# Optimization experiments

Hardware: AMD Instinct MI355X
Metric: run time of the kernel (lower is better)

## Reference

```python
import jax, jax.numpy as jnp
import numpy as np
import math

CHUNK = 64

def _linear(x, W, b):
    # torch nn.Linear: y = x @ W.T + b
    return jnp.einsum('bsd,ed->bse', x, W) + b

def setup_inputs() -> dict:
    key = jax.random.key(0)
    ks = jax.random.split(key, 10)
    B, S, D = 4, 4096, 512
    scale = 0.02
    inp = {
        'x': jax.random.normal(ks[0], (B, S, D), jnp.float32),
        'base_phases': jax.random.normal(ks[1], (S, D), jnp.float32) * math.pi,
        'Wk': jax.random.normal(ks[2], (D, D), jnp.float32) * scale,
        'bk': jnp.zeros((D,), jnp.float32),
        'Wv': jax.random.normal(ks[3], (D, D), jnp.float32) * scale,
        'bv': jnp.zeros((D,), jnp.float32),
        'Wq': jax.random.normal(ks[4], (D, D), jnp.float32) * scale,
        'bq': jnp.zeros((D,), jnp.float32),
        'Wkm': jax.random.normal(ks[5], (D, D), jnp.float32) * scale,
        'bkm': jnp.zeros((D,), jnp.float32),
        'Wqm': jax.random.normal(ks[6], (D, D), jnp.float32) * scale,
        'bqm': jnp.zeros((D,), jnp.float32),
        'mod_scale': jnp.ones((1,), jnp.float32) * 0.1,
        'ln_g': jnp.ones((D,), jnp.float32),
        'ln_b': jnp.zeros((D,), jnp.float32),
        'Wo': jax.random.normal(ks[7], (D, D), jnp.float32) * scale,
        'bo': jnp.zeros((D,), jnp.float32),
    }
    return inp

def reference(x, base_phases, Wk, bk, Wv, bv, Wq, bq, Wkm, bkm, Wqm, bqm, mod_scale, ln_g, ln_b, Wo, bo):
    B, S, D = x.shape
    bp = base_phases[:S][None]                      # [1,S,D]
    key = _linear(x, Wk, bk)
    value = _linear(x, Wv, bv)
    query = _linear(x, Wq, bq)
    key_phase = bp + _linear(key, Wkm, bkm) * mod_scale
    query_phase = bp + _linear(query, Wqm, bqm) * mod_scale
    bound_real = value * jnp.cos(key_phase)
    bound_imag = value * jnp.sin(key_phase)
    # chunked cumulative memory (S divisible by CHUNK -> no padding)
    nC = S // CHUNK
    br = bound_real.reshape(B, nC, CHUNK, D)
    bi = bound_imag.reshape(B, nC, CHUNK, D)
    qp = query_phase.reshape(B, nC, CHUNK, D)
    mem_real = jnp.cumsum(br, axis=2)
    mem_imag = jnp.cumsum(bi, axis=2)
    retrieved = (mem_real * jnp.cos(qp) + mem_imag * jnp.sin(qp)).reshape(B, S, D)
    retrieved = retrieved / math.sqrt(D)
    # LayerNorm + Linear (to_out)
    mu = jnp.mean(retrieved, axis=-1, keepdims=True)
    var = jnp.mean((retrieved - mu) ** 2, axis=-1, keepdims=True)
    normed = (retrieved - mu) / jnp.sqrt(var + 1e-5) * ln_g + ln_b
    out = _linear(normed, Wo, bo)
    return x + out
```

## Files before the change

### kernel.cpp

```cpp
#include <hip/hip_runtime.h>
#include <hip/hip_bf16.h>


typedef __attribute__((ext_vector_type(8))) short short8;
typedef __attribute__((ext_vector_type(4))) float f32x4;

#define M_TOK   16384
#define DIM     512
#define NCHUNK  64
#define RPAD    520

__device__ __forceinline__ void gll16(const void* g, void* l) {
  __builtin_amdgcn_global_load_lds(
      (const __attribute__((address_space(1))) unsigned int*)g,
      (__attribute__((address_space(3))) unsigned int*)l, 16, 0, 0);
}

__device__ __forceinline__ uint2 pack4bf(float4 v) {
  union { __hip_bfloat16 h[4]; uint2 u; } t;
  t.h[0] = __float2bfloat16(v.x);
  t.h[1] = __float2bfloat16(v.y);
  t.h[2] = __float2bfloat16(v.z);
  t.h[3] = __float2bfloat16(v.w);
  return t.u;
}

__global__ __launch_bounds__(256) void prep_all(
    const float* __restrict__ x, __hip_bfloat16* __restrict__ x_bf,
    const float* __restrict__ Wv, const float* __restrict__ Wo,
    const float* __restrict__ bv,
    const float* __restrict__ Wkm, const float* __restrict__ Wqm,
    const float* __restrict__ Wk, const float* __restrict__ Wq,
    const float* __restrict__ bk, const float* __restrict__ bkm,
    const float* __restrict__ bq, const float* __restrict__ bqm,
    __hip_bfloat16* __restrict__ Wall, float* __restrict__ bc1,
    __hip_bfloat16* __restrict__ Wm_bf, __hip_bfloat16* __restrict__ WT_bf) {
  const int tid = threadIdx.x;
  if (blockIdx.x < 8192) {
    int i = blockIdx.x * 256 + tid;
    ((uint2*)x_bf)[i] = pack4bf(((const float4*)x)[i]);
    return;
  }
  const int b = blockIdx.x - 8192;
  if (b < 512) {
    int m = b >> 8;
    int idx = ((b & 255) * 256 + tid) * 4;
    const float* src = m ? Wo : Wv;
    __hip_bfloat16* dst = Wall + (m ? (size_t)1536 * 512 : 0);
    ((uint2*)dst)[idx >> 2] = pack4bf(*(const float4*)(src + idx));
    int t = b * 256 + tid;
    if (t < 512) bc1[t] = bv[t];
  } else if (b < 1024) {
    int bb = b - 512;
    int m = bb >> 8;
    int idx = ((bb & 255) * 256 + tid) * 4;
    const float* src = m ? Wqm : Wkm;
    ((uint2*)(Wm_bf + (size_t)m * 262144))[idx >> 2] =
        pack4bf(*(const float4*)(src + idx));
  } else if (b < 1152) {
    __shared__ float tile[64][65];
    int bb = b - 1024;
    int z = bb >> 6;
    int tl = bb & 63;
    int tr = tl >> 3, tc = tl & 7;
    const float* src = z ? Wq : Wk;
#pragma unroll
    for (int i = 0; i < 4; i++) {
      int r = (tid >> 4) + 16 * i;
      int c4 = (tid & 15) * 4;
      float4 v = *(const float4*)(src + (size_t)(tr * 64 + r) * 512 +
                                  tc * 64 + c4);
      tile[r][c4 + 0] = v.x;
      tile[r][c4 + 1] = v.y;
      tile[r][c4 + 2] = v.z;
      tile[r][c4 + 3] = v.w;
    }
    __syncthreads();
    int orow = tid >> 2;
    int seg = tid & 3;
    __hip_bfloat16* dst = WT_bf + (size_t)z * 262144 +
                          (size_t)(tc * 64 + orow) * 512 + tr * 64 + seg * 16;
#pragma unroll
    for (int q = 0; q < 4; q++) {
      float4 v;
      v.x = tile[seg * 16 + q * 4 + 0][orow];
      v.y = tile[seg * 16 + q * 4 + 1][orow];
      v.z = tile[seg * 16 + q * 4 + 2][orow];
      v.w = tile[seg * 16 + q * 4 + 3][orow];
      *(uint2*)(dst + q * 4) = pack4bf(v);
    }
  } else {
    int row = (b - 1152) * 4 + (tid >> 6);
    int lane = tid & 63;
    int z = row >> 9;
    int i = row & 511;
    const float* Wm = z ? Wqm : Wkm;
    const float* b0 = z ? bq : bk;
    const float* bm = z ? bqm : bkm;
    const float4* w4 = (const float4*)(Wm + (size_t)i * 512 + lane * 8);
    const float4* v4 = (const float4*)(b0 + lane * 8);
    float4 w0 = w4[0], w1 = w4[1], c0 = v4[0], c1 = v4[1];
    float acc = w0.x * c0.x + w0.y * c0.y + w0.z * c0.z + w0.w * c0.w +
                w1.x * c1.x + w1.y * c1.y + w1.z * c1.z + w1.w * c1.w;
#pragma unroll
    for (int off = 32; off; off >>= 1) acc += __shfl_xor(acc, off, 64);
    if (lane == 0) bc1[512 + z * 512 + i] = acc + bm[i];
  }
}

__global__ __launch_bounds__(256) void gemm_bt(
    const __hip_bfloat16* __restrict__ A, int lda,
    const __hip_bfloat16* __restrict__ Bt,
    const float* __restrict__ bias,
    __hip_bfloat16* __restrict__ Cout, int ldc) {
  constexpr int K = 512, BK = 32;
  __shared__ __align__(16) __hip_bfloat16 As[128 * BK];
  __shared__ __align__(16) __hip_bfloat16 Bs[128 * BK];

  const int tid  = threadIdx.x;
  const int lane = tid & 63;
  const int w    = tid >> 6;
  const int wm   = w >> 1;
  const int wn   = w & 1;
  const int m0   = blockIdx.y * 128;
  const int n0   = blockIdx.x * 128;

  const int rS0    = (w * 2 + 0) * 16 + (lane >> 2);
  const int rS1    = (w * 2 + 1) * 16 + (lane >> 2);
  const int kInRow = (lane & 3) * 8;
  const __hip_bfloat16* gA0 = A + (size_t)(m0 + rS0) * lda + kInRow;
  const __hip_bfloat16* gA1 = A + (size_t)(m0 + rS1) * lda + kInRow;
  const __hip_bfloat16* gB0 = Bt + (size_t)(n0 + rS0) * K + kInRow;
  const __hip_bfloat16* gB1 = Bt + (size_t)(n0 + rS1) * K + kInRow;
  char* ldsA0 = (char*)As + (w * 2 + 0) * 1024;
  char* ldsA1 = (char*)As + (w * 2 + 1) * 1024;
  char* ldsB0 = (char*)Bs + (w * 2 + 0) * 1024;
  char* ldsB1 = (char*)Bs + (w * 2 + 1) * 1024;

  f32x4 acc[4][4] = {};

  const int rfA = lane & 15;
  const int rfK = (lane >> 4) * 8;

  for (int kt = 0; kt < K; kt += BK) {
    __syncthreads();
    gll16(gA0 + kt, ldsA0);
    gll16(gA1 + kt, ldsA1);
    gll16(gB0 + kt, ldsB0);
    gll16(gB1 + kt, ldsB1);
    __syncthreads();

    short8 af[4], bf[4];
#pragma unroll
    for (int i = 0; i < 4; i++)
      af[i] = *(const short8*)(As + (wm * 64 + i * 16 + rfA) * BK + rfK);
#pragma unroll
    for (int j = 0; j < 4; j++)
      bf[j] = *(const short8*)(Bs + (wn * 64 + j * 16 + rfA) * BK + rfK);
#pragma unroll
    for (int i = 0; i < 4; i++)
#pragma unroll
      for (int j = 0; j < 4; j++)
        acc[i][j] = __builtin_amdgcn_mfma_f32_16x16x32_bf16(
            af[i], bf[j], acc[i][j], 0, 0, 0);
  }

  const int cq = lane >> 4;
#pragma unroll
  for (int i = 0; i < 4; i++) {
    int row = m0 + wm * 64 + i * 16 + cq * 4;
#pragma unroll
    for (int j = 0; j < 4; j++) {
      int col = n0 + wn * 64 + j * 16 + (lane & 15);
      float bz = bias[col];
#pragma unroll
      for (int r = 0; r < 4; r++) {
        float v = acc[i][j][r] + bz;
        Cout[(size_t)(row + r) * ldc + col] = __float2bfloat16(v);
      }
    }
  }
}

__global__ __launch_bounds__(256) void gemm_compose(
    const __hip_bfloat16* __restrict__ Wm_bf,
    const __hip_bfloat16* __restrict__ WT_bf,
    __hip_bfloat16* __restrict__ Wall) {
  constexpr int K = 512, BK = 32;
  const __hip_bfloat16* A  = Wm_bf + (size_t)blockIdx.z * 262144;
  const __hip_bfloat16* Bt = WT_bf + (size_t)blockIdx.z * 262144;
  __hip_bfloat16* C = Wall + (size_t)(512 + blockIdx.z * 512) * 512;
  __shared__ __align__(16) __hip_bfloat16 As[128 * BK];
  __shared__ __align__(16) __hip_bfloat16 Bs[128 * BK];

  const int tid  = threadIdx.x;
  const int lane = tid & 63;
  const int w    = tid >> 6;
  const int wm   = w >> 1;
  const int wn   = w & 1;
  const int m0   = blockIdx.y * 128;
  const int n0   = blockIdx.x * 128;

  const int rS0    = (w * 2 + 0) * 16 + (lane >> 2);
  const int rS1    = (w * 2 + 1) * 16 + (lane >> 2);
  const int kInRow = (lane & 3) * 8;
  const __hip_bfloat16* gA0 = A + (size_t)(m0 + rS0) * K + kInRow;
  const __hip_bfloat16* gA1 = A + (size_t)(m0 + rS1) * K + kInRow;
  const __hip_bfloat16* gB0 = Bt + (size_t)(n0 + rS0) * K + kInRow;
  const __hip_bfloat16* gB1 = Bt + (size_t)(n0 + rS1) * K + kInRow;
  char* ldsA0 = (char*)As + (w * 2 + 0) * 1024;
  char* ldsA1 = (char*)As + (w * 2 + 1) * 1024;
  char* ldsB0 = (char*)Bs + (w * 2 + 0) * 1024;
  char* ldsB1 = (char*)Bs + (w * 2 + 1) * 1024;

  f32x4 acc[4][4] = {};
  const int rfA = lane & 15;
  const int rfK = (lane >> 4) * 8;

  for (int kt = 0; kt < K; kt += BK) {
    __syncthreads();
    gll16(gA0 + kt, ldsA0);
    gll16(gA1 + kt, ldsA1);
    gll16(gB0 + kt, ldsB0);
    gll16(gB1 + kt, ldsB1);
    __syncthreads();

    short8 af[4], bf[4];
#pragma unroll
    for (int i = 0; i < 4; i++)
      af[i] = *(const short8*)(As + (wm * 64 + i * 16 + rfA) * BK + rfK);
#pragma unroll
    for (int j = 0; j < 4; j++)
      bf[j] = *(const short8*)(Bs + (wn * 64 + j * 16 + rfA) * BK + rfK);
#pragma unroll
    for (int i = 0; i < 4; i++)
#pragma unroll
      for (int j = 0; j < 4; j++)
        acc[i][j] = __builtin_amdgcn_mfma_f32_16x16x32_bf16(
            af[i], bf[j], acc[i][j], 0, 0, 0);
  }

  const int cq = lane >> 4;
#pragma unroll
  for (int i = 0; i < 4; i++) {
    int row = m0 + wm * 64 + i * 16 + cq * 4;
#pragma unroll
    for (int j = 0; j < 4; j++) {
      int col = n0 + wn * 64 + j * 16 + (lane & 15);
#pragma unroll
      for (int r = 0; r < 4; r++)
        C[(size_t)(row + r) * 512 + col] = __float2bfloat16(acc[i][j][r]);
    }
  }
}

__global__ __launch_bounds__(512) void fused_pg(
    const __hip_bfloat16* __restrict__ VKQ,
    const float* __restrict__ bp,
    const float* __restrict__ mod_scale,
    const float* __restrict__ ln_g, const float* __restrict__ ln_b,
    const __hip_bfloat16* __restrict__ WoB,
    const float* __restrict__ bo,
    const float* __restrict__ x,
    float* __restrict__ out) {
  __shared__ __hip_bfloat16 R[64 * RPAD];
  const int tid    = threadIdx.x;
  const int blk    = blockIdx.x;
  const int token0 = blk * 64;
  const int sg0    = (blk & (NCHUNK - 1)) * 64;
  const float msc  = mod_scale[0];
  const float inv_sqrt_d = 0.044194173824159216f;

  {
    const int d = tid;
    float mr = 0.f, mi = 0.f;
    const __hip_bfloat16* vb = VKQ + (size_t)token0 * 1536 + d;
    const float* bb = bp + (size_t)sg0 * 512 + d;
#pragma unroll 4
    for (int s = 0; s < 64; ++s) {
      float v  = __bfloat162float(vb[(size_t)s * 1536]);
      float km = __bfloat162float(vb[(size_t)s * 1536 + 512]);
      float qm = __bfloat162float(vb[(size_t)s * 1536 + 1024]);
      float b  = bb[(size_t)s * 512];
      float kp = b + km * msc;
      float qp = b + qm * msc;
      float sk, ck, sq, cq;
      __sincosf(kp, &sk, &ck);
      __sincosf(qp, &sq, &cq);
      mr += v * ck;
      mi += v * sk;
      R[s * RPAD + d] = __float2bfloat16((mr * cq + mi * sq) * inv_sqrt_d);
    }
  }
  __syncthreads();

  {
    const int lane = tid & 63;
    const int wv   = tid >> 6;
    float gj[8], bj[8];
#pragma unroll
    for (int j = 0; j < 8; j++) {
      int col = lane + 64 * j;
      gj[j] = ln_g[col];
      bj[j] = ln_b[col];
    }
    for (int rr = 0; rr < 8; ++rr) {
      int row = wv * 8 + rr;
      float vals[8], sum = 0.f, sq2 = 0.f;
#pragma unroll
      for (int j = 0; j < 8; j++) {
        float v = __bfloat162float(R[row * RPAD + lane + 64 * j]);
        vals[j] = v;
        sum += v;
        sq2 += v * v;
      }
#pragma unroll
      for (int off = 32; off; off >>= 1) {
        sum += __shfl_xor(sum, off, 64);
        sq2 += __shfl_xor(sq2, off, 64);
      }
      float mu   = sum * (1.f / 512.f);
      float var  = sq2 * (1.f / 512.f) - mu * mu;
      float rstd = rsqrtf(var + 1e-5f);
#pragma unroll
      for (int j = 0; j < 8; j++) {
        float nv = (vals[j] - mu) * rstd * gj[j] + bj[j];
        R[row * RPAD + lane + 64 * j] = __float2bfloat16(nv);
      }
    }
  }
  __syncthreads();

  {
    const int lane = tid & 63;
    const int w    = tid >> 6;
    const int rfA  = lane & 15;
    const int rfK  = (lane >> 4) * 8;
    f32x4 acc[4][4] = {};

    for (int kt = 0; kt < 512; kt += 32) {
      short8 af[4], bf[4];
#pragma unroll
      for (int j = 0; j < 4; j++) {
        int col = w * 64 + j * 16 + rfA;
        bf[j] = *(const short8*)(WoB + (size_t)col * 512 + kt + rfK);
      }
#pragma unroll
      for (int i = 0; i < 4; i++)
        af[i] = *(const short8*)(R + (i * 16 + rfA) * RPAD + kt + rfK);
#pragma unroll
      for (int i = 0; i < 4; i++)
#pragma unroll
        for (int j = 0; j < 4; j++)
          acc[i][j] = __builtin_amdgcn_mfma_f32_16x16x32_bf16(
              af[i], bf[j], acc[i][j], 0, 0, 0);
    }

    const int cq = lane >> 4;
    float bz[4];
#pragma unroll
    for (int j = 0; j < 4; j++) bz[j] = bo[w * 64 + j * 16 + (lane & 15)];
#pragma unroll
    for (int i = 0; i < 4; i++) {
      int row = token0 + i * 16 + cq * 4;
#pragma unroll
      for (int j = 0; j < 4; j++) {
        int col = w * 64 + j * 16 + (lane & 15);
#pragma unroll
        for (int r = 0; r < 4; r++) {
          size_t o = (size_t)(row + r) * 512 + col;
          out[o] = acc[i][j][r] + bz[j] + x[o];
        }
      }
    }
  }
}

extern "C" void kernel_launch(void* const* d_in, const int* in_sizes, int n_in,
                              void* d_out, int out_size, void* d_ws,
                              size_t ws_size, hipStream_t stream) {
  const float* x    = (const float*)d_in[0];
  const float* bp   = (const float*)d_in[1];
  const float* Wk   = (const float*)d_in[2];
  const float* bk   = (const float*)d_in[3];
  const float* Wv   = (const float*)d_in[4];
  const float* bv   = (const float*)d_in[5];
  const float* Wq   = (const float*)d_in[6];
  const float* bq   = (const float*)d_in[7];
  const float* Wkm  = (const float*)d_in[8];
  const float* bkm  = (const float*)d_in[9];
  const float* Wqm  = (const float*)d_in[10];
  const float* bqm  = (const float*)d_in[11];
  const float* msc  = (const float*)d_in[12];
  const float* lng  = (const float*)d_in[13];
  const float* lnb  = (const float*)d_in[14];
  const float* Wo   = (const float*)d_in[15];
  const float* bo   = (const float*)d_in[16];
  float* out = (float*)d_out;

  char* ws = (char*)d_ws;
  __hip_bfloat16* x_bf  = (__hip_bfloat16*)ws;  ws += (size_t)M_TOK * DIM * 2;
  __hip_bfloat16* Wall  = (__hip_bfloat16*)ws;  ws += (size_t)2048 * 512 * 2;
  __hip_bfloat16* Wm_bf = (__hip_bfloat16*)ws;  ws += (size_t)2 * 262144 * 2;
  __hip_bfloat16* WT_bf = (__hip_bfloat16*)ws;  ws += (size_t)2 * 262144 * 2;
  float*          bc1   = (float*)ws;           ws += 1536 * 4;
  __hip_bfloat16* VKQ   = (__hip_bfloat16*)ws;  ws += (size_t)M_TOK * 1536 * 2;

  prep_all<<<9600, 256, 0, stream>>>(x, x_bf, Wv, Wo, bv, Wkm, Wqm, Wk, Wq,
                                     bk, bkm, bq, bqm, Wall, bc1, Wm_bf,
                                     WT_bf);
  gemm_compose<<<dim3(4, 4, 2), 256, 0, stream>>>(Wm_bf, WT_bf, Wall);
  gemm_bt<<<dim3(12, 128), 256, 0, stream>>>(x_bf, DIM, Wall, bc1, VKQ, 1536);
  fused_pg<<<256, 512, 0, stream>>>(VKQ, bp, msc, lng, lnb,
                                    Wall + (size_t)1536 * 512, bo, x, out);
}
```

Baseline: 221.7 us.

## Split chunk cumsum across two thread segments with carry fix-up, 1024-thread blocks

The fused phase/LayerNorm/output kernel now runs 1024 threads per block. The 64-token chunk scan is split into two 32-token halves that run in parallel. The first half's running totals go to shared memory, and the second half's rows are then corrected by adding that carry rotated by the query phase. LayerNorm rows and the output-GEMM column tiles are redistributed across the 16 waves. This halves the serial scan length on a grid of only 256 blocks, at the cost of an extra pass with another sincos per element, extra bf16 rounding of the intermediate, and higher register pressure under the 1024-thread launch bound.

```diff
diff --git a/kernel.cpp b/kernel.cpp
--- a/kernel.cpp
+++ b/kernel.cpp
@@ -254,7 +254,7 @@
   }
 }
 
-__global__ __launch_bounds__(512) void fused_pg(
+__global__ __launch_bounds__(1024) void fused_pg(
     const __hip_bfloat16* __restrict__ VKQ,
     const float* __restrict__ bp,
     const float* __restrict__ mod_scale,
@@ -264,20 +264,23 @@
     const float* __restrict__ x,
     float* __restrict__ out) {
   __shared__ __hip_bfloat16 R[64 * RPAD];
+  __shared__ float Tr[512], Ti[512];
   const int tid    = threadIdx.x;
+  const int seg    = tid >> 9;
+  const int d      = tid & 511;
   const int blk    = blockIdx.x;
   const int token0 = blk * 64;
   const int sg0    = (blk & (NCHUNK - 1)) * 64;
   const float msc  = mod_scale[0];
-  const float inv_sqrt_d = 0.044194173824159216f;
+  const float isd  = 0.044194173824159216f;
 
   {
-    const int d = tid;
+    const int s0 = seg * 32;
     float mr = 0.f, mi = 0.f;
-    const __hip_bfloat16* vb = VKQ + (size_t)token0 * 1536 + d;
-    const float* bb = bp + (size_t)sg0 * 512 + d;
+    const __hip_bfloat16* vb = VKQ + (size_t)(token0 + s0) * 1536 + d;
+    const float* bb = bp + (size_t)(sg0 + s0) * 512 + d;
 #pragma unroll 4
-    for (int s = 0; s < 64; ++s) {
+    for (int s = 0; s < 32; ++s) {
       float v  = __bfloat162float(vb[(size_t)s * 1536]);
       float km = __bfloat162float(vb[(size_t)s * 1536 + 512]);
       float qm = __bfloat162float(vb[(size_t)s * 1536 + 1024]);
@@ -289,7 +292,31 @@
       __sincosf(qp, &sq, &cq);
       mr += v * ck;
       mi += v * sk;
-      R[s * RPAD + d] = __float2bfloat16((mr * cq + mi * sq) * inv_sqrt_d);
+      R[(s0 + s) * RPAD + d] = __float2bfloat16((mr * cq + mi * sq) * isd);
+    }
+    if (seg == 0) {
+      Tr[d] = mr;
+      Ti[d] = mi;
+    }
+  }
+  __syncthreads();
+
+  {
+    const int r0 = 32 + seg * 16;
+    const float pr = Tr[d] * isd;
+    const float pi = Ti[d] * isd;
+    const __hip_bfloat16* qb = VKQ + (size_t)(token0 + r0) * 1536 + 1024 + d;
+    const float* bb = bp + (size_t)(sg0 + r0) * 512 + d;
+#pragma unroll 4
+    for (int s = 0; s < 16; ++s) {
+      float qm = __bfloat162float(qb[(size_t)s * 1536]);
+      float b  = bb[(size_t)s * 512];
+      float qp = b + qm * msc;
+      float sq, cq;
+      __sincosf(qp, &sq, &cq);
+      int idx = (r0 + s) * RPAD + d;
+      float v = __bfloat162float(R[idx]) + pr * cq + pi * sq;
+      R[idx] = __float2bfloat16(v);
     }
   }
   __syncthreads();
@@ -304,8 +331,8 @@
       gj[j] = ln_g[col];
       bj[j] = ln_b[col];
     }
-    for (int rr = 0; rr < 8; ++rr) {
-      int row = wv * 8 + rr;
+    for (int rr = 0; rr < 4; ++rr) {
+      int row = wv * 4 + rr;
       float vals[8], sum = 0.f, sq2 = 0.f;
 #pragma unroll
       for (int j = 0; j < 8; j++) {
@@ -336,13 +363,13 @@
     const int w    = tid >> 6;
     const int rfA  = lane & 15;
     const int rfK  = (lane >> 4) * 8;
-    f32x4 acc[4][4] = {};
+    f32x4 acc[4][2] = {};
 
     for (int kt = 0; kt < 512; kt += 32) {
-      short8 af[4], bf[4];
-#pragma unroll
-      for (int j = 0; j < 4; j++) {
-        int col = w * 64 + j * 16 + rfA;
+      short8 af[4], bf[2];
+#pragma unroll
+      for (int j = 0; j < 2; j++) {
+        int col = w * 32 + j * 16 + rfA;
         bf[j] = *(const short8*)(WoB + (size_t)col * 512 + kt + rfK);
       }
 #pragma unroll
@@ -351,21 +378,21 @@
 #pragma unroll
       for (int i = 0; i < 4; i++)
 #pragma unroll
-        for (int j = 0; j < 4; j++)
+        for (int j = 0; j < 2; j++)
           acc[i][j] = __builtin_amdgcn_mfma_f32_16x16x32_bf16(
               af[i], bf[j], acc[i][j], 0, 0, 0);
     }
 
     const int cq = lane >> 4;
-    float bz[4];
-#pragma unroll
-    for (int j = 0; j < 4; j++) bz[j] = bo[w * 64 + j * 16 + (lane & 15)];
+    float bz[2];
+#pragma unroll
+    for (int j = 0; j < 2; j++) bz[j] = bo[w * 32 + j * 16 + (lane & 15)];
 #pragma unroll
     for (int i = 0; i < 4; i++) {
       int row = token0 + i * 16 + cq * 4;
 #pragma unroll
-      for (int j = 0; j < 4; j++) {
-        int col = w * 64 + j * 16 + (lane & 15);
+      for (int j = 0; j < 2; j++) {
+        int col = w * 32 + j * 16 + (lane & 15);
 #pragma unroll
         for (int r = 0; r < 4; r++) {
           size_t o = (size_t)(row + r) * 512 + col;
@@ -411,6 +438,6 @@
                                      WT_bf);
   gemm_compose<<<dim3(4, 4, 2), 256, 0, stream>>>(Wm_bf, WT_bf, Wall);
   gemm_bt<<<dim3(12, 128), 256, 0, stream>>>(x_bf, DIM, Wall, bc1, VKQ, 1536);
-  fused_pg<<<256, 512, 0, stream>>>(VKQ, bp, msc, lng, lnb,
-                                    Wall + (size_t)1536 * 512, bo, x, out);
-}
+  fused_pg<<<256, 1024, 0, stream>>>(VKQ, bp, msc, lng, lnb,
+                                     Wall + (size_t)1536 * 512, bo, x, out);
+}
```

Result: faster. 203.7 us (-8.1%).

## Fuse input projection GEMM into phase/cumsum/LayerNorm/output kernel

Applied to the files above, without the earlier changes.

Removes the separate x-to-bf16 conversion and the large VKQ projection GEMM. Each 1024-thread block now converts its 64 tokens of x into LDS and computes the V, K-phase and Q-phase projections with MFMA directly. The chunk cumsum is done in registers with wave shuffles, and LayerNorm plus the Wo projection run in the same kernel. This avoids writing and re-reading the 16384x1536 bf16 intermediate, at the cost of only 256 blocks, heavy register pressure (the cksk array plus accumulators) and repeated global reads of the weights per block.

```diff
diff --git a/kernel.cpp b/kernel.cpp
--- a/kernel.cpp
+++ b/kernel.cpp
@@ -7,8 +7,7 @@
 
 #define M_TOK   16384
 #define DIM     512
-#define NCHUNK  64
-#define RPAD    520
+#define APAD    520
 
 __device__ __forceinline__ void gll16(const void* g, void* l) {
   __builtin_amdgcn_global_load_lds(
@@ -25,8 +24,21 @@
   return t.u;
 }
 
+__device__ __forceinline__ unsigned packbf2(float a, float b) {
+  union { __hip_bfloat16 h[2]; unsigned u; } t;
+  t.h[0] = __float2bfloat16(a);
+  t.h[1] = __float2bfloat16(b);
+  return t.u;
+}
+
+__device__ __forceinline__ float bflo(unsigned u) {
+  union { unsigned x; float f; } t; t.x = u << 16; return t.f;
+}
+__device__ __forceinline__ float bfhi(unsigned u) {
+  union { unsigned x; float f; } t; t.x = u & 0xffff0000u; return t.f;
+}
+
 __global__ __launch_bounds__(256) void prep_all(
-    const float* __restrict__ x, __hip_bfloat16* __restrict__ x_bf,
     const float* __restrict__ Wv, const float* __restrict__ Wo,
     const float* __restrict__ bv,
     const float* __restrict__ Wkm, const float* __restrict__ Wqm,
@@ -36,12 +48,7 @@
     __hip_bfloat16* __restrict__ Wall, float* __restrict__ bc1,
     __hip_bfloat16* __restrict__ Wm_bf, __hip_bfloat16* __restrict__ WT_bf) {
   const int tid = threadIdx.x;
-  if (blockIdx.x < 8192) {
-    int i = blockIdx.x * 256 + tid;
-    ((uint2*)x_bf)[i] = pack4bf(((const float4*)x)[i]);
-    return;
-  }
-  const int b = blockIdx.x - 8192;
+  const int b = blockIdx.x;
   if (b < 512) {
     int m = b >> 8;
     int idx = ((b & 255) * 256 + tid) * 4;
@@ -63,13 +70,12 @@
     int z = bb >> 6;
     int tl = bb & 63;
     int tr = tl >> 3, tc = tl & 7;
-    const float* src = z ? Wq : Wk;
 #pragma unroll
     for (int i = 0; i < 4; i++) {
       int r = (tid >> 4) + 16 * i;
       int c4 = (tid & 15) * 4;
-      float4 v = *(const float4*)(src + (size_t)(tr * 64 + r) * 512 +
-                                  tc * 64 + c4);
+      float4 v = *(const float4*)((z ? Wq : Wk) +
+                                  (size_t)(tr * 64 + r) * 512 + tc * 64 + c4);
       tile[r][c4 + 0] = v.x;
       tile[r][c4 + 1] = v.y;
       tile[r][c4 + 2] = v.z;
@@ -81,13 +87,13 @@
     __hip_bfloat16* dst = WT_bf + (size_t)z * 262144 +
                           (size_t)(tc * 64 + orow) * 512 + tr * 64 + seg * 16;
 #pragma unroll
-    for (int q = 0; q < 4; q++) {
+    for (int qq = 0; qq < 4; qq++) {
       float4 v;
-      v.x = tile[seg * 16 + q * 4 + 0][orow];
-      v.y = tile[seg * 16 + q * 4 + 1][orow];
-      v.z = tile[seg * 16 + q * 4 + 2][orow];
-      v.w = tile[seg * 16 + q * 4 + 3][orow];
-      *(uint2*)(dst + q * 4) = pack4bf(v);
+      v.x = tile[seg * 16 + qq * 4 + 0][orow];
+      v.y = tile[seg * 16 + qq * 4 + 1][orow];
+      v.z = tile[seg * 16 + qq * 4 + 2][orow];
+      v.w = tile[seg * 16 + qq * 4 + 3][orow];
+      *(uint2*)(dst + qq * 4) = pack4bf(v);
     }
   } else {
     int row = (b - 1152) * 4 + (tid >> 6);
@@ -108,80 +114,6 @@
   }
 }
 
-__global__ __launch_bounds__(256) void gemm_bt(
-    const __hip_bfloat16* __restrict__ A, int lda,
-    const __hip_bfloat16* __restrict__ Bt,
-    const float* __restrict__ bias,
-    __hip_bfloat16* __restrict__ Cout, int ldc) {
-  constexpr int K = 512, BK = 32;
-  __shared__ __align__(16) __hip_bfloat16 As[128 * BK];
-  __shared__ __align__(16) __hip_bfloat16 Bs[128 * BK];
-
-  const int tid  = threadIdx.x;
-  const int lane = tid & 63;
-  const int w    = tid >> 6;
-  const int wm   = w >> 1;
-  const int wn   = w & 1;
-  const int m0   = blockIdx.y * 128;
-  const int n0   = blockIdx.x * 128;
-
-  const int rS0    = (w * 2 + 0) * 16 + (lane >> 2);
-  const int rS1    = (w * 2 + 1) * 16 + (lane >> 2);
-  const int kInRow = (lane & 3) * 8;
-  const __hip_bfloat16* gA0 = A + (size_t)(m0 + rS0) * lda + kInRow;
-  const __hip_bfloat16* gA1 = A + (size_t)(m0 + rS1) * lda + kInRow;
-  const __hip_bfloat16* gB0 = Bt + (size_t)(n0 + rS0) * K + kInRow;
-  const __hip_bfloat16* gB1 = Bt + (size_t)(n0 + rS1) * K + kInRow;
-  char* ldsA0 = (char*)As + (w * 2 + 0) * 1024;
-  char* ldsA1 = (char*)As + (w * 2 + 1) * 1024;
-  char* ldsB0 = (char*)Bs + (w * 2 + 0) * 1024;
-  char* ldsB1 = (char*)Bs + (w * 2 + 1) * 1024;
-
-  f32x4 acc[4][4] = {};
-
-  const int rfA = lane & 15;
-  const int rfK = (lane >> 4) * 8;
-
-  for (int kt = 0; kt < K; kt += BK) {
-    __syncthreads();
-    gll16(gA0 + kt, ldsA0);
-    gll16(gA1 + kt, ldsA1);
-    gll16(gB0 + kt, ldsB0);
-    gll16(gB1 + kt, ldsB1);
-    __syncthreads();
-
-    short8 af[4], bf[4];
-#pragma unroll
-    for (int i = 0; i < 4; i++)
-      af[i] = *(const short8*)(As + (wm * 64 + i * 16 + rfA) * BK + rfK);
-#pragma unroll
-    for (int j = 0; j < 4; j++)
-      bf[j] = *(const short8*)(Bs + (wn * 64 + j * 16 + rfA) * BK + rfK);
-#pragma unroll
-    for (int i = 0; i < 4; i++)
-#pragma unroll
-      for (int j = 0; j < 4; j++)
-        acc[i][j] = __builtin_amdgcn_mfma_f32_16x16x32_bf16(
-            af[i], bf[j], acc[i][j], 0, 0, 0);
-  }
-
-  const int cq = lane >> 4;
-#pragma unroll
-  for (int i = 0; i < 4; i++) {
-    int row = m0 + wm * 64 + i * 16 + cq * 4;
-#pragma unroll
-    for (int j = 0; j < 4; j++) {
-      int col = n0 + wn * 64 + j * 16 + (lane & 15);
-      float bz = bias[col];
-#pragma unroll
-      for (int r = 0; r < 4; r++) {
-        float v = acc[i][j][r] + bz;
-        Cout[(size_t)(row + r) * ldc + col] = __float2bfloat16(v);
-      }
-    }
-  }
-}
-
 __global__ __launch_bounds__(256) void gemm_compose(
     const __hip_bfloat16* __restrict__ Wm_bf,
     const __hip_bfloat16* __restrict__ WT_bf,
@@ -254,49 +186,148 @@
   }
 }
 
-__global__ __launch_bounds__(512) void fused_pg(
-    const __hip_bfloat16* __restrict__ VKQ,
+__device__ __forceinline__ void mfma_pass(
+    const __hip_bfloat16* __restrict__ Alds,
+    const __hip_bfloat16* __restrict__ Bt,
+    int c, int q, int d0, f32x4 acc[4][2]) {
+  const int rfK = q * 8;
+  for (int kt = 0; kt < 512; kt += 32) {
+    short8 af[4], bf[2];
+#pragma unroll
+    for (int j = 0; j < 2; j++)
+      bf[j] = *(const short8*)(Bt + (size_t)(d0 + 16 * j) * 512 + kt + rfK);
+#pragma unroll
+    for (int i = 0; i < 4; i++)
+      af[i] = *(const short8*)(Alds + (i * 16 + c) * APAD + kt + rfK);
+#pragma unroll
+    for (int i = 0; i < 4; i++)
+#pragma unroll
+      for (int j = 0; j < 2; j++)
+        acc[i][j] = __builtin_amdgcn_mfma_f32_16x16x32_bf16(
+            af[i], bf[j], acc[i][j], 0, 0, 0);
+  }
+}
+
+__global__ __launch_bounds__(1024) void fused_all(
+    const float* __restrict__ x,
+    const __hip_bfloat16* __restrict__ Wall,
+    const float* __restrict__ bc1,
     const float* __restrict__ bp,
     const float* __restrict__ mod_scale,
     const float* __restrict__ ln_g, const float* __restrict__ ln_b,
-    const __hip_bfloat16* __restrict__ WoB,
     const float* __restrict__ bo,
-    const float* __restrict__ x,
     float* __restrict__ out) {
-  __shared__ __hip_bfloat16 R[64 * RPAD];
+  __shared__ __hip_bfloat16 At[64 * APAD];
+  __shared__ __hip_bfloat16 R[64 * APAD];
   const int tid    = threadIdx.x;
-  const int blk    = blockIdx.x;
-  const int token0 = blk * 64;
-  const int sg0    = (blk & (NCHUNK - 1)) * 64;
+  const int lane   = tid & 63;
+  const int wv     = tid >> 6;
+  const int q      = lane >> 4;
+  const int c      = lane & 15;
+  const int token0 = blockIdx.x * 64;
+  const int sg0    = (blockIdx.x & 63) * 64;
   const float msc  = mod_scale[0];
-  const float inv_sqrt_d = 0.044194173824159216f;
-
-  {
-    const int d = tid;
-    float mr = 0.f, mi = 0.f;
-    const __hip_bfloat16* vb = VKQ + (size_t)token0 * 1536 + d;
-    const float* bb = bp + (size_t)sg0 * 512 + d;
-#pragma unroll 4
-    for (int s = 0; s < 64; ++s) {
-      float v  = __bfloat162float(vb[(size_t)s * 1536]);
-      float km = __bfloat162float(vb[(size_t)s * 1536 + 512]);
-      float qm = __bfloat162float(vb[(size_t)s * 1536 + 1024]);
-      float b  = bb[(size_t)s * 512];
-      float kp = b + km * msc;
-      float qp = b + qm * msc;
-      float sk, ck, sq, cq;
-      __sincosf(kp, &sk, &ck);
-      __sincosf(qp, &sq, &cq);
-      mr += v * ck;
-      mi += v * sk;
-      R[s * RPAD + d] = __float2bfloat16((mr * cq + mi * sq) * inv_sqrt_d);
+  const float isd  = 0.044194173824159216f;
+  const int d0     = wv * 32 + c;
+
+  {
+    const float4* xs = (const float4*)(x + (size_t)token0 * 512);
+#pragma unroll
+    for (int kc = 0; kc < 8; kc++) {
+      int idx = kc * 1024 + tid;
+      int row = idx >> 7;
+      int col4 = idx & 127;
+      *(uint2*)((char*)At + row * (APAD * 2) + col4 * 8) = pack4bf(xs[idx]);
     }
   }
   __syncthreads();
 
   {
-    const int lane = tid & 63;
-    const int wv   = tid >> 6;
+    f32x4 acc[4][2] = {};
+    mfma_pass(At, Wall + (size_t)1024 * 512, c, q, d0, acc);
+    float bq0 = bc1[1024 + d0], bq1 = bc1[1024 + d0 + 16];
+#pragma unroll
+    for (int i = 0; i < 4; i++)
+#pragma unroll
+      for (int r = 0; r < 4; r++) {
+        int s = i * 16 + q * 4 + r;
+        const float* bprow = bp + (size_t)(sg0 + s) * 512;
+        R[s * APAD + d0] =
+            __float2bfloat16(bprow[d0] + (acc[i][0][r] + bq0) * msc);
+        R[s * APAD + d0 + 16] =
+            __float2bfloat16(bprow[d0 + 16] + (acc[i][1][r] + bq1) * msc);
+      }
+  }
+
+  unsigned cksk[4][2][4];
+  {
+    f32x4 acc[4][2] = {};
+    mfma_pass(At, Wall + (size_t)512 * 512, c, q, d0, acc);
+    float bk0 = bc1[512 + d0], bk1 = bc1[512 + d0 + 16];
+#pragma unroll
+    for (int i = 0; i < 4; i++)
+#pragma unroll
+      for (int r = 0; r < 4; r++) {
+        int s = i * 16 + q * 4 + r;
+        const float* bprow = bp + (size_t)(sg0 + s) * 512;
+        float kp0 = bprow[d0] + (acc[i][0][r] + bk0) * msc;
+        float kp1 = bprow[d0 + 16] + (acc[i][1][r] + bk1) * msc;
+        float s0, c0, s1, c1;
+        __sincosf(kp0, &s0, &c0);
+        __sincosf(kp1, &s1, &c1);
+        cksk[i][0][r] = packbf2(c0, s0);
+        cksk[i][1][r] = packbf2(c1, s1);
+      }
+  }
+
+  {
+    f32x4 acc[4][2] = {};
+    mfma_pass(At, Wall, c, q, d0, acc);
+    float bv0 = bc1[d0], bv1 = bc1[d0 + 16];
+#pragma unroll
+    for (int j = 0; j < 2; j++) {
+      const int d = d0 + 16 * j;
+      const float bvj = j ? bv1 : bv0;
+      float carry_r = 0.f, carry_i = 0.f;
+#pragma unroll
+      for (int i = 0; i < 4; i++) {
+        float br[4], bi[4];
+#pragma unroll
+        for (int r = 0; r < 4; r++) {
+          float v = acc[i][j][r] + bvj;
+          unsigned pk = cksk[i][j][r];
+          br[r] = v * bflo(pk);
+          bi[r] = v * bfhi(pk);
+        }
+        br[1] += br[0]; br[2] += br[1]; br[3] += br[2];
+        bi[1] += bi[0]; bi[2] += bi[1]; bi[3] += bi[2];
+        float Sr = br[3], Si = bi[3];
+        float s0r = __shfl(Sr, c, 64),      s0i = __shfl(Si, c, 64);
+        float s1r = __shfl(Sr, 16 + c, 64), s1i = __shfl(Si, 16 + c, 64);
+        float s2r = __shfl(Sr, 32 + c, 64), s2i = __shfl(Si, 32 + c, 64);
+        float s3r = __shfl(Sr, 48 + c, 64), s3i = __shfl(Si, 48 + c, 64);
+        float Er = (q > 0 ? s0r : 0.f) + (q > 1 ? s1r : 0.f) +
+                   (q > 2 ? s2r : 0.f);
+        float Ei = (q > 0 ? s0i : 0.f) + (q > 1 ? s1i : 0.f) +
+                   (q > 2 ? s2i : 0.f);
+#pragma unroll
+        for (int r = 0; r < 4; r++) {
+          float mr = br[r] + Er + carry_r;
+          float mi = bi[r] + Ei + carry_i;
+          int s = i * 16 + q * 4 + r;
+          float qp = __bfloat162float(R[s * APAD + d]);
+          float sq, cq2;
+          __sincosf(qp, &sq, &cq2);
+          R[s * APAD + d] = __float2bfloat16((mr * cq2 + mi * sq) * isd);
+        }
+        carry_r += s0r + s1r + s2r + s3r;
+        carry_i += s0i + s1i + s2i + s3i;
+      }
+    }
+  }
+  __syncthreads();
+
+  {
     float gj[8], bj[8];
 #pragma unroll
     for (int j = 0; j < 8; j++) {
@@ -304,12 +335,12 @@
       gj[j] = ln_g[col];
       bj[j] = ln_b[col];
     }
-    for (int rr = 0; rr < 8; ++rr) {
-      int row = wv * 8 + rr;
+    for (int rr = 0; rr < 4; ++rr) {
+      int row = wv * 4 + rr;
       float vals[8], sum = 0.f, sq2 = 0.f;
 #pragma unroll
       for (int j = 0; j < 8; j++) {
-        float v = __bfloat162float(R[row * RPAD + lane + 64 * j]);
+        float v = __bfloat162float(R[row * APAD + lane + 64 * j]);
         vals[j] = v;
         sum += v;
         sq2 += v * v;
@@ -325,54 +356,29 @@
 #pragma unroll
       for (int j = 0; j < 8; j++) {
         float nv = (vals[j] - mu) * rstd * gj[j] + bj[j];
-        R[row * RPAD + lane + 64 * j] = __float2bfloat16(nv);
+        R[row * APAD + lane + 64 * j] = __float2bfloat16(nv);
       }
     }
   }
   __syncthreads();
 
   {
-    const int lane = tid & 63;
-    const int w    = tid >> 6;
-    const int rfA  = lane & 15;
-    const int rfK  = (lane >> 4) * 8;
-    f32x4 acc[4][4] = {};
-
-    for (int kt = 0; kt < 512; kt += 32) {
-      short8 af[4], bf[4];
-#pragma unroll
-      for (int j = 0; j < 4; j++) {
-        int col = w * 64 + j * 16 + rfA;
-        bf[j] = *(const short8*)(WoB + (size_t)col * 512 + kt + rfK);
-      }
-#pragma unroll
-      for (int i = 0; i < 4; i++)
-        af[i] = *(const short8*)(R + (i * 16 + rfA) * RPAD + kt + rfK);
-#pragma unroll
-      for (int i = 0; i < 4; i++)
-#pragma unroll
-        for (int j = 0; j < 4; j++)
-          acc[i][j] = __builtin_amdgcn_mfma_f32_16x16x32_bf16(
-              af[i], bf[j], acc[i][j], 0, 0, 0);
-    }
-
-    const int cq = lane >> 4;
-    float bz[4];
-#pragma unroll
-    for (int j = 0; j < 4; j++) bz[j] = bo[w * 64 + j * 16 + (lane & 15)];
-#pragma unroll
-    for (int i = 0; i < 4; i++) {
-      int row = token0 + i * 16 + cq * 4;
-#pragma unroll
-      for (int j = 0; j < 4; j++) {
-        int col = w * 64 + j * 16 + (lane & 15);
+    f32x4 acc[4][2] = {};
+    mfma_pass(R, Wall + (size_t)1536 * 512, c, q, d0, acc);
+    float bz0 = bo[d0], bz1 = bo[d0 + 16];
+#pragma unroll
+    for (int i = 0; i < 4; i++)
+#pragma unroll
+      for (int j = 0; j < 2; j++) {
+        int col = d0 + 16 * j;
+        float bz = j ? bz1 : bz0;
 #pragma unroll
         for (int r = 0; r < 4; r++) {
-          size_t o = (size_t)(row + r) * 512 + col;
-          out[o] = acc[i][j][r] + bz[j] + x[o];
+          int row = token0 + i * 16 + q * 4 + r;
+          size_t o = (size_t)row * 512 + col;
+          out[o] = acc[i][j][r] + bz + x[o];
         }
       }
-    }
   }
 }
 
@@ -399,18 +405,14 @@
   float* out = (float*)d_out;
 
   char* ws = (char*)d_ws;
-  __hip_bfloat16* x_bf  = (__hip_bfloat16*)ws;  ws += (size_t)M_TOK * DIM * 2;
   __hip_bfloat16* Wall  = (__hip_bfloat16*)ws;  ws += (size_t)2048 * 512 * 2;
   __hip_bfloat16* Wm_bf = (__hip_bfloat16*)ws;  ws += (size_t)2 * 262144 * 2;
   __hip_bfloat16* WT_bf = (__hip_bfloat16*)ws;  ws += (size_t)2 * 262144 * 2;
   float*          bc1   = (float*)ws;           ws += 1536 * 4;
-  __hip_bfloat16* VKQ   = (__hip_bfloat16*)ws;  ws += (size_t)M_TOK * 1536 * 2;
-
-  prep_all<<<9600, 256, 0, stream>>>(x, x_bf, Wv, Wo, bv, Wkm, Wqm, Wk, Wq,
-                                     bk, bkm, bq, bqm, Wall, bc1, Wm_bf,
-                                     WT_bf);
+
+  prep_all<<<1408, 256, 0, stream>>>(Wv, Wo, bv, Wkm, Wqm, Wk, Wq, bk, bkm,
+                                     bq, bqm, Wall, bc1, Wm_bf, WT_bf);
   gemm_compose<<<dim3(4, 4, 2), 256, 0, stream>>>(Wm_bf, WT_bf, Wall);
-  gemm_bt<<<dim3(12, 128), 256, 0, stream>>>(x_bf, DIM, Wall, bc1, VKQ, 1536);
-  fused_pg<<<256, 512, 0, stream>>>(VKQ, bp, msc, lng, lnb,
-                                    Wall + (size_t)1536 * 512, bo, x, out);
-}
+  fused_all<<<256, 1024, 0, stream>>>(x, Wall, bc1, bp, msc, lng, lnb, bo,
+                                      out);
+}
```

After: 230.7 us. 1.04x slower.
